# Performance work log

Measured on AMD Instinct MI355X. Metric: run time of the kernel, lower is better.

## Reference

```python
import jax, jax.numpy as jnp
import numpy as np

H = 16       # num_heads
DH = 64      # dim_head
SCALE = DH ** -0.5


def setup_inputs() -> dict:
    key = jax.random.key(0)
    k1, k2 = jax.random.split(key)
    ZT = jax.random.normal(k1, (2, 2048, 1024), dtype=jnp.float32)
    # Linear weight, shape (H*dh, dim); scaled like a typical init for stability
    W = jax.random.normal(k2, (1024, 1024), dtype=jnp.float32) * 0.02
    return {"ZT": ZT, "W": W}


def reference(ZT, W):
    b, n, dim = ZT.shape
    # UT(ZT): ZT @ W^T -> (b, n, H*dh), reshape to (b, h, n, dh)
    ZTU = jnp.einsum('bnd,ed->bne', ZT, W).reshape(b, n, H, DH).transpose(0, 2, 1, 3)
    # scores = ZTU @ ZTU^T * scale  (b, h, n, n)
    scores = jnp.einsum('bhnd,bhmd->bhnm', ZTU, ZTU) * SCALE
    attn = jax.nn.softmax(scores, axis=-1)  # dropout p=0 -> identity
    # attn @ ZTU -> (b, h, n, dh) -> (b, n, H*dh)
    ssa = jnp.einsum('bhnm,bhmd->bhnd', attn, ZTU)
    ssa = ssa.transpose(0, 2, 1, 3).reshape(b, n, H * DH)
    # UT(I).T == W (shape (H*dh, dim)); final projection back to dim
    mssa = jnp.einsum('bne,ed->bnd', ssa, W)
    # return_proj=False path: module returns (MSSA_out, MSSA_out)
    return (mssa, mssa)
```

## Files before the change

kernel.cpp:

```cpp
#include <hip/hip_runtime.h>
#include <hip/hip_bf16.h>
#include <stdint.h>

typedef __attribute__((ext_vector_type(8))) short bf16x8;
typedef __attribute__((ext_vector_type(4))) float f32x4;

#define MFMA16(a, b, c) __builtin_amdgcn_mfma_f32_16x16x32_bf16(a, b, c, 0, 0, 0)

typedef const __attribute__((address_space(1))) unsigned int* as1_u32p;
typedef __attribute__((address_space(3))) unsigned int* as3_u32p;
__device__ __forceinline__ void gl_lds16(const void* g, void* l) {
    __builtin_amdgcn_global_load_lds((as1_u32p)g, (as3_u32p)l, 16, 0, 0);
}

__device__ __forceinline__ unsigned short f2bs(float f) {
    __hip_bfloat16 h = __float2bfloat16(f);
    unsigned short s;
    __builtin_memcpy(&s, &h, 2);
    return s;
}

__device__ __forceinline__ unsigned int pk_bf16(float a, float b) {
    float2 f; f.x = a; f.y = b;
    __hip_bfloat162 h = __float22bfloat162_rn(f);
    unsigned int u;
    __builtin_memcpy(&u, &h, 4);
    return u;
}

__device__ __forceinline__ float exp2_raw(float x) {
    float r;
    asm("v_exp_f32 %0, %1" : "=v"(r) : "v"(x));
    return r;
}

#define QSCALE 0.18033688f

__global__ __launch_bounds__(256) void cvt_k(const float* __restrict__ zt,
                                             const float* __restrict__ w,
                                             unsigned short* __restrict__ ztbf,
                                             unsigned short* __restrict__ wbf,
                                             unsigned short* __restrict__ wtbf) {
    __shared__ __attribute__((aligned(16))) unsigned short T[64 * 72];
    const int bid = blockIdx.x;
    const int tid = threadIdx.x;
    if (bid < 4096) {
        int i = bid * 256 + tid;
        const float4 v = ((const float4*)zt)[i];
        ushort4 p;
        p.x = f2bs(v.x); p.y = f2bs(v.y); p.z = f2bs(v.z); p.w = f2bs(v.w);
        ((ushort4*)ztbf)[i] = p;
    } else {
        const int b2 = bid - 4096;
        const int e0 = (b2 >> 4) * 64, d0 = (b2 & 15) * 64;
        const int el = tid >> 2;
        const int dl = (tid & 3) * 16;
        const float* src = w + (size_t)(e0 + el) * 1024 + d0 + dl;
        unsigned short myv[16];
#pragma unroll
        for (int q = 0; q < 4; ++q) {
            const float4 v = *(const float4*)(src + q * 4);
            myv[q * 4 + 0] = f2bs(v.x);
            myv[q * 4 + 1] = f2bs(v.y);
            myv[q * 4 + 2] = f2bs(v.z);
            myv[q * 4 + 3] = f2bs(v.w);
        }
        *(bf16x8*)(wbf + (size_t)(e0 + el) * 1024 + d0 + dl) = *(const bf16x8*)&myv[0];
        *(bf16x8*)(wbf + (size_t)(e0 + el) * 1024 + d0 + dl + 8) = *(const bf16x8*)&myv[8];
        const int epl = 4 * (el & 15) + (el >> 4);
#pragma unroll
        for (int q = 0; q < 16; ++q) T[(dl + q) * 72 + epl] = myv[q];
        __syncthreads();
#pragma unroll
        for (int p = 0; p < 2; ++p) {
            const int idx = p * 256 + tid;
            const int dd = idx >> 3, c = (idx & 7) * 8;
            const bf16x8 v = *(const bf16x8*)&T[dd * 72 + c];
            *(bf16x8*)(wtbf + (size_t)(d0 + dd) * 1024 + e0 + c) = v;
        }
    }
}

template <int EPI>
__global__ __launch_bounds__(256, 2) void gemm_bt_k(
    const __hip_bfloat16* __restrict__ A, const __hip_bfloat16* __restrict__ B, int K,
    unsigned short* __restrict__ ztu, unsigned short* __restrict__ ztut,
    float* __restrict__ out0, float* __restrict__ out1) {
    __shared__ __attribute__((aligned(16))) unsigned short smem[12288];
    unsigned short* At = smem;
    unsigned short* Bt = smem + 4096;
    unsigned short* Tb = smem;

    const int bn = blockIdx.x, bm = blockIdx.y;
    const int tid = threadIdx.x;
    const int wave = tid >> 6, lane = tid & 63;
    const int wm = wave >> 1, wn = wave & 1;
    const int quad = lane >> 4, l16 = lane & 15;

    f32x4 acc[2][4] = {};

    const int lr = lane >> 2, lc = (lane & 3) * 8;
    const __hip_bfloat16* Ag = A + (size_t)(bm * 64 + wave * 16 + lr) * K + lc;
    const __hip_bfloat16* Bg0 = B + (size_t)(bn * 128 + (2 * wave) * 16 + lr) * K + lc;
    const __hip_bfloat16* Bg1 = B + (size_t)(bn * 128 + (2 * wave + 1) * 16 + lr) * K + lc;
    unsigned short* lA = At + wave * 512;
    unsigned short* lB0 = Bt + (2 * wave) * 512;
    unsigned short* lB1 = Bt + (2 * wave + 1) * 512;

    const int nk = K >> 6;
    for (int kt = 0; kt < nk; ++kt) {
        const int ko = kt << 6;
        gl_lds16(Ag + ko, lA);
        gl_lds16(Ag + ko + 32, lA + 2048);
        gl_lds16(Bg0 + ko, lB0);
        gl_lds16(Bg0 + ko + 32, lB0 + 4096);
        gl_lds16(Bg1 + ko, lB1);
        gl_lds16(Bg1 + ko + 32, lB1 + 4096);
        __syncthreads();
        bf16x8 af[2][2], bfr[2][4];
#pragma unroll
        for (int h = 0; h < 2; ++h)
#pragma unroll
            for (int i = 0; i < 2; ++i)
                af[h][i] = *(const bf16x8*)&At[h * 2048 + (wm * 32 + i * 16 + l16) * 32 + quad * 8];
#pragma unroll
        for (int h = 0; h < 2; ++h)
#pragma unroll
            for (int j = 0; j < 4; ++j)
                bfr[h][j] = *(const bf16x8*)&Bt[h * 4096 + (wn * 64 + j * 16 + l16) * 32 + quad * 8];
#pragma unroll
        for (int h = 0; h < 2; ++h)
#pragma unroll
            for (int i = 0; i < 2; ++i)
#pragma unroll
                for (int j = 0; j < 4; ++j) acc[i][j] = MFMA16(af[h][i], bfr[h][j], acc[i][j]);
        __syncthreads();
    }

    if (EPI == 0) {
        const int h = bn * 2 + wn;
        const int bb = bm >> 5;
        const int nb = (bm & 31) * 64;
        const size_t hb = (size_t)(bb * 16 + h) * 131072;
#pragma unroll
        for (int i = 0; i < 2; ++i) {
#pragma unroll
            for (int r = 0; r < 4; ++r) {
                const int n = nb + wm * 32 + i * 16 + quad * 4 + r;
                uint2 pk;
                pk.x = pk_bf16(acc[i][0][r], acc[i][1][r]);
                pk.y = pk_bf16(acc[i][2][r], acc[i][3][r]);
                *(uint2*)(ztu + hb + n * 64 + l16 * 4) = pk;
                const int npl = 16 * quad + 4 * r + 2 * wm + i;
                Tb[(wn * 64 + 0 + l16) * 72 + npl] = (unsigned short)(pk.x & 0xffff);
                Tb[(wn * 64 + 16 + l16) * 72 + npl] = (unsigned short)(pk.x >> 16);
                Tb[(wn * 64 + 32 + l16) * 72 + npl] = (unsigned short)(pk.y & 0xffff);
                Tb[(wn * 64 + 48 + l16) * 72 + npl] = (unsigned short)(pk.y >> 16);
            }
        }
        __syncthreads();
#pragma unroll
        for (int ee = 0; ee < 4; ++ee) {
            const int e_local = wave * 32 + ee * 8 + (lane >> 3);
            const int nc = (lane & 7) * 8;
            const bf16x8 v = *(const bf16x8*)&Tb[e_local * 72 + nc];
            const int hh = bn * 2 + (e_local >> 6);
            const int dh = e_local & 63;
            *(bf16x8*)(ztut + (size_t)(bb * 16 + hh) * 131072 + dh * 2048 + nb + nc) = v;
        }
    } else {
#pragma unroll
        for (int i = 0; i < 2; ++i) {
#pragma unroll
            for (int r = 0; r < 4; ++r) {
                const int mm = bm * 64 + wm * 32 + i * 16 + quad * 4 + r;
#pragma unroll
                for (int j = 0; j < 4; ++j) {
                    const int e = bn * 128 + wn * 64 + j * 16 + l16;
                    const float v = acc[i][j][r];
                    out0[(size_t)mm * 1024 + e] = v;
                    out1[(size_t)mm * 1024 + e] = v;
                }
            }
        }
    }
}

__global__ __launch_bounds__(512, 4) void attn_k(const unsigned short* __restrict__ ztu,
                                                 const unsigned short* __restrict__ ztut,
                                                 unsigned short* __restrict__ ssa) {
    __shared__ __attribute__((aligned(16))) unsigned short Kt[64 * 64];
    __shared__ __attribute__((aligned(16))) unsigned short Vt[64 * 64];
    __shared__ __attribute__((aligned(16))) unsigned short Pt[8][16 * 72];
    const int qt = blockIdx.x, bh = blockIdx.y;
    const int tid = threadIdx.x, wave = tid >> 6, lane = tid & 63;
    const int quad = lane >> 4, l16 = lane & 15;
    const unsigned short* base = ztu + (size_t)bh * 131072;
    const unsigned short* baseT = ztut + (size_t)bh * 131072;

    const int qb = qt * 128 + wave * 16;
    const bf16x8 qa0 = *(const bf16x8*)(base + (qb + l16) * 64 + quad * 8);
    const bf16x8 qa1 = *(const bf16x8*)(base + (qb + l16) * 64 + 32 + quad * 8);

    float lsum[4] = {};
    f32x4 o[4] = {};

    const int lrow = lane >> 3;
    const int sw = (lane & 7) ^ lrow;
    const unsigned short* gK = base + (wave * 8 + lrow) * 64 + sw * 8;
    const unsigned short* gV = baseT + (size_t)(wave * 8 + lrow) * 2048 + sw * 8;
    unsigned short* lK = &Kt[wave * 512];
    unsigned short* lV = &Vt[wave * 512];
    unsigned short* pw = &Pt[wave][0];

    const int swq = (quad ^ (l16 & 7));
    const int koff0 = l16 * 64 + swq * 8;
    const int koff1 = l16 * 64 + (swq ^ 4) * 8;

    for (int t = 0; t < 32; ++t) {
        gl_lds16(gK + t * 4096, lK);
        gl_lds16(gV + t * 64, lV);
        __syncthreads();

        f32x4 s[4];
#pragma unroll
        for (int nf = 0; nf < 4; ++nf) {
            bf16x8 kb0 = *(const bf16x8*)&Kt[nf * 1024 + koff0];
            bf16x8 kb1 = *(const bf16x8*)&Kt[nf * 1024 + koff1];
            f32x4 z = {0.f, 0.f, 0.f, 0.f};
            z = MFMA16(qa0, kb0, z);
            z = MFMA16(qa1, kb1, z);
            s[nf] = z;
        }

#pragma unroll
        for (int r = 0; r < 4; ++r) {
            const float p0 = exp2_raw(s[0][r] * QSCALE);
            const float p1 = exp2_raw(s[1][r] * QSCALE);
            const float p2 = exp2_raw(s[2][r] * QSCALE);
            const float p3 = exp2_raw(s[3][r] * QSCALE);
            lsum[r] += (p0 + p1) + (p2 + p3);
            uint2 pk;
            pk.x = pk_bf16(p0, p1);
            pk.y = pk_bf16(p2, p3);
            *(uint2*)&pw[(quad * 4 + r) * 72 + l16 * 4] = pk;
        }
        asm volatile("s_waitcnt lgkmcnt(0)" ::: "memory");

        bf16x8 pa0 = *(const bf16x8*)&pw[l16 * 72 + quad * 8];
        bf16x8 pa1 = *(const bf16x8*)&pw[l16 * 72 + 32 + quad * 8];
#pragma unroll
        for (int df = 0; df < 4; ++df) {
            bf16x8 vb0 = *(const bf16x8*)&Vt[df * 1024 + koff0];
            bf16x8 vb1 = *(const bf16x8*)&Vt[df * 1024 + koff1];
            o[df] = MFMA16(pa0, vb0, o[df]);
            o[df] = MFMA16(pa1, vb1, o[df]);
        }
        __syncthreads();
    }

    const int b = bh >> 4, h = bh & 15;
#pragma unroll
    for (int r = 0; r < 4; ++r) {
        float v = lsum[r];
        v += __shfl_xor(v, 1);
        v += __shfl_xor(v, 2);
        v += __shfl_xor(v, 4);
        v += __shfl_xor(v, 8);
        const float inv = 1.0f / v;
        const int token = b * 2048 + qt * 128 + wave * 16 + quad * 4 + r;
        uint2 pk;
        pk.x = pk_bf16(o[0][r] * inv, o[1][r] * inv);
        pk.y = pk_bf16(o[2][r] * inv, o[3][r] * inv);
        *(uint2*)(ssa + (size_t)token * 1024 + h * 64 + l16 * 4) = pk;
    }
}

extern "C" void kernel_launch(void* const* d_in, const int* in_sizes, int n_in,
                              void* d_out, int out_size, void* d_ws, size_t ws_size,
                              hipStream_t stream) {
    const float* ZT = (const float*)d_in[0];
    const float* W = (const float*)d_in[1];
    float* out = (float*)d_out;
    char* ws = (char*)d_ws;

    unsigned short* ztbf  = (unsigned short*)(ws);
    unsigned short* wbf   = (unsigned short*)(ws + 8u * 1024 * 1024);
    unsigned short* wtbf  = (unsigned short*)(ws + 10u * 1024 * 1024);
    unsigned short* ztu   = (unsigned short*)(ws + 12u * 1024 * 1024);
    unsigned short* ztut  = (unsigned short*)(ws + 20u * 1024 * 1024);
    unsigned short* ssabf = (unsigned short*)(ws + 28u * 1024 * 1024);

    cvt_k<<<4352, 256, 0, stream>>>(ZT, W, ztbf, wbf, wtbf);
    gemm_bt_k<0><<<dim3(8, 64), 256, 0, stream>>>((const __hip_bfloat16*)ztbf,
                                                  (const __hip_bfloat16*)wbf, 1024, ztu, ztut,
                                                  nullptr, nullptr);
    attn_k<<<dim3(16, 32), 512, 0, stream>>>(ztu, ztut, ssabf);
    gemm_bt_k<1><<<dim3(8, 64), 256, 0, stream>>>((const __hip_bfloat16*)ssabf,
                                                  (const __hip_bfloat16*)wtbf, 1024, nullptr,
                                                  nullptr, out, out + 4194304);
}
```

Before: 167.2 us.

## Fuse ZT fp32-to-bf16 conversion into GEMM, double attention rows per wave, swizzle grids

The first GEMM now reads ZT in fp32 and converts it to bf16 while filling LDS, so the separate ZT conversion pass and its workspace round trip go away. The attention kernel moves from 8 waves of 16 query rows each to 4 waves of 32 rows, so every K/V fragment read from LDS feeds twice as many MFMAs. Both kernels also switch to 1D grids with remapped block indices to group tiles that share data. In exchange, the A-tile loads in the first GEMM become synchronous register loads instead of direct global-to-LDS copies, and the attention kernel uses more registers per wave with fewer waves per block.

```diff
diff --git a/kernel.cpp b/kernel.cpp
--- a/kernel.cpp
+++ b/kernel.cpp
@@ -36,54 +36,44 @@
 
 #define QSCALE 0.18033688f
 
-__global__ __launch_bounds__(256) void cvt_k(const float* __restrict__ zt,
-                                             const float* __restrict__ w,
-                                             unsigned short* __restrict__ ztbf,
-                                             unsigned short* __restrict__ wbf,
-                                             unsigned short* __restrict__ wtbf) {
+__global__ __launch_bounds__(256) void cvt_w_k(const float* __restrict__ w,
+                                               unsigned short* __restrict__ wbf,
+                                               unsigned short* __restrict__ wtbf) {
     __shared__ __attribute__((aligned(16))) unsigned short T[64 * 72];
-    const int bid = blockIdx.x;
+    const int b2 = blockIdx.x;
     const int tid = threadIdx.x;
-    if (bid < 4096) {
-        int i = bid * 256 + tid;
-        const float4 v = ((const float4*)zt)[i];
-        ushort4 p;
-        p.x = f2bs(v.x); p.y = f2bs(v.y); p.z = f2bs(v.z); p.w = f2bs(v.w);
-        ((ushort4*)ztbf)[i] = p;
-    } else {
-        const int b2 = bid - 4096;
-        const int e0 = (b2 >> 4) * 64, d0 = (b2 & 15) * 64;
-        const int el = tid >> 2;
-        const int dl = (tid & 3) * 16;
-        const float* src = w + (size_t)(e0 + el) * 1024 + d0 + dl;
-        unsigned short myv[16];
-#pragma unroll
-        for (int q = 0; q < 4; ++q) {
-            const float4 v = *(const float4*)(src + q * 4);
-            myv[q * 4 + 0] = f2bs(v.x);
-            myv[q * 4 + 1] = f2bs(v.y);
-            myv[q * 4 + 2] = f2bs(v.z);
-            myv[q * 4 + 3] = f2bs(v.w);
-        }
-        *(bf16x8*)(wbf + (size_t)(e0 + el) * 1024 + d0 + dl) = *(const bf16x8*)&myv[0];
-        *(bf16x8*)(wbf + (size_t)(e0 + el) * 1024 + d0 + dl + 8) = *(const bf16x8*)&myv[8];
-        const int epl = 4 * (el & 15) + (el >> 4);
-#pragma unroll
-        for (int q = 0; q < 16; ++q) T[(dl + q) * 72 + epl] = myv[q];
-        __syncthreads();
-#pragma unroll
-        for (int p = 0; p < 2; ++p) {
-            const int idx = p * 256 + tid;
-            const int dd = idx >> 3, c = (idx & 7) * 8;
-            const bf16x8 v = *(const bf16x8*)&T[dd * 72 + c];
-            *(bf16x8*)(wtbf + (size_t)(d0 + dd) * 1024 + e0 + c) = v;
-        }
+    const int e0 = (b2 >> 4) * 64, d0 = (b2 & 15) * 64;
+    const int el = tid >> 2;
+    const int dl = (tid & 3) * 16;
+    const float* src = w + (size_t)(e0 + el) * 1024 + d0 + dl;
+    unsigned short myv[16];
+#pragma unroll
+    for (int q = 0; q < 4; ++q) {
+        const float4 v = *(const float4*)(src + q * 4);
+        myv[q * 4 + 0] = f2bs(v.x);
+        myv[q * 4 + 1] = f2bs(v.y);
+        myv[q * 4 + 2] = f2bs(v.z);
+        myv[q * 4 + 3] = f2bs(v.w);
+    }
+    *(bf16x8*)(wbf + (size_t)(e0 + el) * 1024 + d0 + dl) = *(const bf16x8*)&myv[0];
+    *(bf16x8*)(wbf + (size_t)(e0 + el) * 1024 + d0 + dl + 8) = *(const bf16x8*)&myv[8];
+    const int epl = 4 * (el & 15) + (el >> 4);
+#pragma unroll
+    for (int q = 0; q < 16; ++q) T[(dl + q) * 72 + epl] = myv[q];
+    __syncthreads();
+#pragma unroll
+    for (int p = 0; p < 2; ++p) {
+        const int idx = p * 256 + tid;
+        const int dd = idx >> 3, c = (idx & 7) * 8;
+        const bf16x8 v = *(const bf16x8*)&T[dd * 72 + c];
+        *(bf16x8*)(wtbf + (size_t)(d0 + dd) * 1024 + e0 + c) = v;
     }
 }
 
 template <int EPI>
 __global__ __launch_bounds__(256, 2) void gemm_bt_k(
-    const __hip_bfloat16* __restrict__ A, const __hip_bfloat16* __restrict__ B, int K,
+    const float* __restrict__ Af32, const __hip_bfloat16* __restrict__ Abf,
+    const __hip_bfloat16* __restrict__ B,
     unsigned short* __restrict__ ztu, unsigned short* __restrict__ ztut,
     float* __restrict__ out0, float* __restrict__ out1) {
     __shared__ __attribute__((aligned(16))) unsigned short smem[12288];
@@ -91,7 +81,9 @@
     unsigned short* Bt = smem + 4096;
     unsigned short* Tb = smem;
 
-    const int bn = blockIdx.x, bm = blockIdx.y;
+    const int p = blockIdx.x;
+    const int bm = (p & 7) * 8 + ((p >> 3) & 7);
+    const int bn = p >> 6;
     const int tid = threadIdx.x;
     const int wave = tid >> 6, lane = tid & 63;
     const int wm = wave >> 1, wn = wave & 1;
@@ -100,18 +92,33 @@
     f32x4 acc[2][4] = {};
 
     const int lr = lane >> 2, lc = (lane & 3) * 8;
-    const __hip_bfloat16* Ag = A + (size_t)(bm * 64 + wave * 16 + lr) * K + lc;
-    const __hip_bfloat16* Bg0 = B + (size_t)(bn * 128 + (2 * wave) * 16 + lr) * K + lc;
-    const __hip_bfloat16* Bg1 = B + (size_t)(bn * 128 + (2 * wave + 1) * 16 + lr) * K + lc;
+    const float* Agf = Af32 ? Af32 + (size_t)(bm * 64 + wave * 16 + lr) * 1024 + lc : nullptr;
+    const __hip_bfloat16* Agb =
+        Abf ? Abf + (size_t)(bm * 64 + wave * 16 + lr) * 1024 + lc : nullptr;
+    const __hip_bfloat16* Bg0 = B + (size_t)(bn * 128 + (2 * wave) * 16 + lr) * 1024 + lc;
+    const __hip_bfloat16* Bg1 = B + (size_t)(bn * 128 + (2 * wave + 1) * 16 + lr) * 1024 + lc;
     unsigned short* lA = At + wave * 512;
     unsigned short* lB0 = Bt + (2 * wave) * 512;
     unsigned short* lB1 = Bt + (2 * wave + 1) * 512;
 
-    const int nk = K >> 6;
-    for (int kt = 0; kt < nk; ++kt) {
+    for (int kt = 0; kt < 16; ++kt) {
         const int ko = kt << 6;
-        gl_lds16(Ag + ko, lA);
-        gl_lds16(Ag + ko + 32, lA + 2048);
+        if (EPI == 0) {
+#pragma unroll
+            for (int h = 0; h < 2; ++h) {
+                const float4 v0 = *(const float4*)(Agf + ko + h * 32);
+                const float4 v1 = *(const float4*)(Agf + ko + h * 32 + 4);
+                uint4 wv;
+                wv.x = pk_bf16(v0.x, v0.y);
+                wv.y = pk_bf16(v0.z, v0.w);
+                wv.z = pk_bf16(v1.x, v1.y);
+                wv.w = pk_bf16(v1.z, v1.w);
+                *(uint4*)(lA + h * 2048 + lr * 32 + lc) = wv;
+            }
+        } else {
+            gl_lds16(Agb + ko, lA);
+            gl_lds16(Agb + ko + 32, lA + 2048);
+        }
         gl_lds16(Bg0 + ko, lB0);
         gl_lds16(Bg0 + ko + 32, lB0 + 4096);
         gl_lds16(Bg1 + ko, lB1);
@@ -186,31 +193,43 @@
     }
 }
 
-__global__ __launch_bounds__(512, 4) void attn_k(const unsigned short* __restrict__ ztu,
+__global__ __launch_bounds__(256, 4) void attn_k(const unsigned short* __restrict__ ztu,
                                                  const unsigned short* __restrict__ ztut,
                                                  unsigned short* __restrict__ ssa) {
     __shared__ __attribute__((aligned(16))) unsigned short Kt[64 * 64];
     __shared__ __attribute__((aligned(16))) unsigned short Vt[64 * 64];
-    __shared__ __attribute__((aligned(16))) unsigned short Pt[8][16 * 72];
-    const int qt = blockIdx.x, bh = blockIdx.y;
+    __shared__ __attribute__((aligned(16))) unsigned short Pt[4][32 * 72];
+    const int p = blockIdx.x;
+    const int ii = p >> 3;
+    const int bh = (p & 7) * 4 + (ii >> 4);
+    const int qt = ii & 15;
     const int tid = threadIdx.x, wave = tid >> 6, lane = tid & 63;
     const int quad = lane >> 4, l16 = lane & 15;
     const unsigned short* base = ztu + (size_t)bh * 131072;
     const unsigned short* baseT = ztut + (size_t)bh * 131072;
 
-    const int qb = qt * 128 + wave * 16;
-    const bf16x8 qa0 = *(const bf16x8*)(base + (qb + l16) * 64 + quad * 8);
-    const bf16x8 qa1 = *(const bf16x8*)(base + (qb + l16) * 64 + 32 + quad * 8);
-
-    float lsum[4] = {};
-    f32x4 o[4] = {};
-
+    const int qb = qt * 128 + wave * 32;
+    bf16x8 qa[2][2];
+#pragma unroll
+    for (int g = 0; g < 2; ++g) {
+        qa[g][0] = *(const bf16x8*)(base + (qb + g * 16 + l16) * 64 + quad * 8);
+        qa[g][1] = *(const bf16x8*)(base + (qb + g * 16 + l16) * 64 + 32 + quad * 8);
+    }
+
+    float lsum[2][4] = {};
+    f32x4 o[2][4] = {};
+
+    const int c0 = wave * 2, c1 = c0 + 1;
     const int lrow = lane >> 3;
     const int sw = (lane & 7) ^ lrow;
-    const unsigned short* gK = base + (wave * 8 + lrow) * 64 + sw * 8;
-    const unsigned short* gV = baseT + (size_t)(wave * 8 + lrow) * 2048 + sw * 8;
-    unsigned short* lK = &Kt[wave * 512];
-    unsigned short* lV = &Vt[wave * 512];
+    const unsigned short* gK0 = base + (c0 * 8 + lrow) * 64 + sw * 8;
+    const unsigned short* gK1 = base + (c1 * 8 + lrow) * 64 + sw * 8;
+    const unsigned short* gV0 = baseT + (size_t)(c0 * 8 + lrow) * 2048 + sw * 8;
+    const unsigned short* gV1 = baseT + (size_t)(c1 * 8 + lrow) * 2048 + sw * 8;
+    unsigned short* lK0 = &Kt[c0 * 512];
+    unsigned short* lK1 = &Kt[c1 * 512];
+    unsigned short* lV0 = &Vt[c0 * 512];
+    unsigned short* lV1 = &Vt[c1 * 512];
     unsigned short* pw = &Pt[wave][0];
 
     const int swq = (quad ^ (l16 & 7));
@@ -218,61 +237,79 @@
     const int koff1 = l16 * 64 + (swq ^ 4) * 8;
 
     for (int t = 0; t < 32; ++t) {
-        gl_lds16(gK + t * 4096, lK);
-        gl_lds16(gV + t * 64, lV);
-        __syncthreads();
-
-        f32x4 s[4];
+        gl_lds16(gK0 + t * 4096, lK0);
+        gl_lds16(gK1 + t * 4096, lK1);
+        gl_lds16(gV0 + t * 64, lV0);
+        gl_lds16(gV1 + t * 64, lV1);
+        __syncthreads();
+
+        f32x4 s[2][4];
 #pragma unroll
         for (int nf = 0; nf < 4; ++nf) {
             bf16x8 kb0 = *(const bf16x8*)&Kt[nf * 1024 + koff0];
             bf16x8 kb1 = *(const bf16x8*)&Kt[nf * 1024 + koff1];
-            f32x4 z = {0.f, 0.f, 0.f, 0.f};
-            z = MFMA16(qa0, kb0, z);
-            z = MFMA16(qa1, kb1, z);
-            s[nf] = z;
-        }
-
-#pragma unroll
-        for (int r = 0; r < 4; ++r) {
-            const float p0 = exp2_raw(s[0][r] * QSCALE);
-            const float p1 = exp2_raw(s[1][r] * QSCALE);
-            const float p2 = exp2_raw(s[2][r] * QSCALE);
-            const float p3 = exp2_raw(s[3][r] * QSCALE);
-            lsum[r] += (p0 + p1) + (p2 + p3);
-            uint2 pk;
-            pk.x = pk_bf16(p0, p1);
-            pk.y = pk_bf16(p2, p3);
-            *(uint2*)&pw[(quad * 4 + r) * 72 + l16 * 4] = pk;
+#pragma unroll
+            for (int g = 0; g < 2; ++g) {
+                f32x4 z = {0.f, 0.f, 0.f, 0.f};
+                z = MFMA16(qa[g][0], kb0, z);
+                z = MFMA16(qa[g][1], kb1, z);
+                s[g][nf] = z;
+            }
+        }
+
+#pragma unroll
+        for (int g = 0; g < 2; ++g) {
+#pragma unroll
+            for (int r = 0; r < 4; ++r) {
+                const float p0 = exp2_raw(s[g][0][r] * QSCALE);
+                const float p1 = exp2_raw(s[g][1][r] * QSCALE);
+                const float p2 = exp2_raw(s[g][2][r] * QSCALE);
+                const float p3 = exp2_raw(s[g][3][r] * QSCALE);
+                lsum[g][r] += (p0 + p1) + (p2 + p3);
+                uint2 pk;
+                pk.x = pk_bf16(p0, p1);
+                pk.y = pk_bf16(p2, p3);
+                *(uint2*)&pw[(g * 16 + quad * 4 + r) * 72 + l16 * 4] = pk;
+            }
         }
         asm volatile("s_waitcnt lgkmcnt(0)" ::: "memory");
 
-        bf16x8 pa0 = *(const bf16x8*)&pw[l16 * 72 + quad * 8];
-        bf16x8 pa1 = *(const bf16x8*)&pw[l16 * 72 + 32 + quad * 8];
+        bf16x8 pa[2][2];
+#pragma unroll
+        for (int g = 0; g < 2; ++g) {
+            pa[g][0] = *(const bf16x8*)&pw[(g * 16 + l16) * 72 + quad * 8];
+            pa[g][1] = *(const bf16x8*)&pw[(g * 16 + l16) * 72 + 32 + quad * 8];
+        }
 #pragma unroll
         for (int df = 0; df < 4; ++df) {
             bf16x8 vb0 = *(const bf16x8*)&Vt[df * 1024 + koff0];
             bf16x8 vb1 = *(const bf16x8*)&Vt[df * 1024 + koff1];
-            o[df] = MFMA16(pa0, vb0, o[df]);
-            o[df] = MFMA16(pa1, vb1, o[df]);
+#pragma unroll
+            for (int g = 0; g < 2; ++g) {
+                o[g][df] = MFMA16(pa[g][0], vb0, o[g][df]);
+                o[g][df] = MFMA16(pa[g][1], vb1, o[g][df]);
+            }
         }
         __syncthreads();
     }
 
     const int b = bh >> 4, h = bh & 15;
 #pragma unroll
-    for (int r = 0; r < 4; ++r) {
-        float v = lsum[r];
-        v += __shfl_xor(v, 1);
-        v += __shfl_xor(v, 2);
-        v += __shfl_xor(v, 4);
-        v += __shfl_xor(v, 8);
-        const float inv = 1.0f / v;
-        const int token = b * 2048 + qt * 128 + wave * 16 + quad * 4 + r;
-        uint2 pk;
-        pk.x = pk_bf16(o[0][r] * inv, o[1][r] * inv);
-        pk.y = pk_bf16(o[2][r] * inv, o[3][r] * inv);
-        *(uint2*)(ssa + (size_t)token * 1024 + h * 64 + l16 * 4) = pk;
+    for (int g = 0; g < 2; ++g) {
+#pragma unroll
+        for (int r = 0; r < 4; ++r) {
+            float v = lsum[g][r];
+            v += __shfl_xor(v, 1);
+            v += __shfl_xor(v, 2);
+            v += __shfl_xor(v, 4);
+            v += __shfl_xor(v, 8);
+            const float inv = 1.0f / v;
+            const int token = b * 2048 + qt * 128 + wave * 32 + g * 16 + quad * 4 + r;
+            uint2 pk;
+            pk.x = pk_bf16(o[g][0][r] * inv, o[g][1][r] * inv);
+            pk.y = pk_bf16(o[g][2][r] * inv, o[g][3][r] * inv);
+            *(uint2*)(ssa + (size_t)token * 1024 + h * 64 + l16 * 4) = pk;
+        }
     }
 }
 
@@ -284,19 +321,17 @@
     float* out = (float*)d_out;
     char* ws = (char*)d_ws;
 
-    unsigned short* ztbf  = (unsigned short*)(ws);
-    unsigned short* wbf   = (unsigned short*)(ws + 8u * 1024 * 1024);
-    unsigned short* wtbf  = (unsigned short*)(ws + 10u * 1024 * 1024);
-    unsigned short* ztu   = (unsigned short*)(ws + 12u * 1024 * 1024);
-    unsigned short* ztut  = (unsigned short*)(ws + 20u * 1024 * 1024);
-    unsigned short* ssabf = (unsigned short*)(ws + 28u * 1024 * 1024);
-
-    cvt_k<<<4352, 256, 0, stream>>>(ZT, W, ztbf, wbf, wtbf);
-    gemm_bt_k<0><<<dim3(8, 64), 256, 0, stream>>>((const __hip_bfloat16*)ztbf,
-                                                  (const __hip_bfloat16*)wbf, 1024, ztu, ztut,
-                                                  nullptr, nullptr);
-    attn_k<<<dim3(16, 32), 512, 0, stream>>>(ztu, ztut, ssabf);
-    gemm_bt_k<1><<<dim3(8, 64), 256, 0, stream>>>((const __hip_bfloat16*)ssabf,
-                                                  (const __hip_bfloat16*)wtbf, 1024, nullptr,
-                                                  nullptr, out, out + 4194304);
-}
+    unsigned short* wbf   = (unsigned short*)(ws);
+    unsigned short* wtbf  = (unsigned short*)(ws + 2u * 1024 * 1024);
+    unsigned short* ztu   = (unsigned short*)(ws + 4u * 1024 * 1024);
+    unsigned short* ztut  = (unsigned short*)(ws + 12u * 1024 * 1024);
+    unsigned short* ssabf = (unsigned short*)(ws + 20u * 1024 * 1024);
+
+    cvt_w_k<<<256, 256, 0, stream>>>(W, wbf, wtbf);
+    gemm_bt_k<0><<<512, 256, 0, stream>>>(ZT, nullptr, (const __hip_bfloat16*)wbf, ztu, ztut,
+                                          nullptr, nullptr);
+    attn_k<<<512, 256, 0, stream>>>(ztu, ztut, ssabf);
+    gemm_bt_k<1><<<512, 256, 0, stream>>>(nullptr, (const __hip_bfloat16*)ssabf,
+                                          (const __hip_bfloat16*)wtbf, nullptr, nullptr, out,
+                                          out + 4194304);
+}
```

Measured after the change: 162.8 us. 2.7% less time.
